# Optimization experiments

Hardware: AMD Instinct MI355X
Metric: run time of the kernel (lower is better)

## Reference

```python
import jax, jax.numpy as jnp
import numpy as np

H, W = 300, 400            # grid_size
RES = 0.1                  # resolution (m/pixel)
X0, X1 = -20.0, 20.0       # x_range
Y0, Y1 = -10.0, 30.0       # y_range
Z0, Z1 = -3.0, 4.0         # z_range
MAX_INT = 255.0            # max_intensity
N_MAX = 128.0              # density_normalize
K_SAMPLES = 512            # >= max Bresenham steps inside grid (diag <= 400)


def _rasterize_polyline(pts_xy):
    """DDA line rasterization of an ego-frame polyline -> [H, W] binary grid.
    Matches the Bresenham + 3x3 stamp (width 2 or 3 -> half_w=1) of the original."""
    px = jnp.trunc((pts_xy[:, 0] - X0) / RES)  # int() truncation as in original
    py = jnp.trunc((pts_xy[:, 1] - Y0) / RES)
    p = jnp.stack([px, py], axis=-1)           # [N, 2] pixel coords (float)
    a, b = p[:-1], p[1:]                        # segment endpoints [S, 2]

    def inb(q):
        return (q[:, 0] >= 0) & (q[:, 0] < W) & (q[:, 1] >= 0) & (q[:, 1] < H)

    valid = inb(a) | inb(b)                     # draw if either endpoint in bounds
    lo = jnp.array([0.0, 0.0], jnp.float32)
    hi = jnp.array([W - 1.0, H - 1.0], jnp.float32)
    a = jnp.clip(a, lo, hi)
    b = jnp.clip(b, lo, hi)

    dmax = jnp.max(jnp.abs(b - a), axis=-1)     # [S] major-axis length in pixels
    k = jnp.arange(K_SAMPLES, dtype=jnp.float32)
    t = jnp.minimum(k[None, :], dmax[:, None]) / jnp.maximum(dmax[:, None], 1.0)
    pts = a[:, None, :] + t[..., None] * (b - a)[:, None, :]   # [S, K, 2]
    pix = jnp.round(pts).astype(jnp.int32)

    offs = jnp.arange(-1, 2)                    # half_w = width//2 = 1 -> 3x3 stamp
    xs = pix[..., 0][..., None, None] + offs[:, None]          # [S, K, 3, 1]
    ys = pix[..., 1][..., None, None] + offs[None, :]          # [S, K, 1, 3]
    xs, ys = jnp.broadcast_arrays(xs, ys)
    val = jnp.broadcast_to(valid.astype(jnp.float32)[:, None, None, None], xs.shape)
    # out-of-bounds stamped pixels are dropped, as in the original bounds check
    return jnp.zeros((H, W), jnp.float32).at[ys, xs].max(val, mode="drop")


def _rasterize_lidar(points):
    """[N,4] (x,y,z,intensity) -> [3,H,W] (height, mean intensity, log density)."""
    x, y, z, inten = points[:, 0], points[:, 1], points[:, 2], points[:, 3]
    mask = (x >= X0) & (x < X1) & (y >= Y0) & (y < Y1)
    px = jnp.clip(((x - X0) / RES).astype(jnp.int32), 0, W - 1)
    py = jnp.clip(((y - Y0) / RES).astype(jnp.int32), 0, H - 1)
    w = mask.astype(jnp.float32)
    neg_inf = jnp.float32(-jnp.inf)

    hmax = jnp.full((H, W), neg_inf, jnp.float32).at[py, px].max(
        jnp.where(mask, z, neg_inf))
    hmax = jnp.where(jnp.isneginf(hmax), 0.0, hmax)  # empty cells -> 0 BEFORE norm

    isum = jnp.zeros((H, W), jnp.float32).at[py, px].add(inten * w)
    cnt = jnp.zeros((H, W), jnp.float32).at[py, px].add(w)
    imean = jnp.where(cnt > 0, isum / jnp.maximum(cnt, 1.0), 0.0)

    h = jnp.clip((hmax - Z0) / (Z1 - Z0), 0.0, 1.0)
    i = jnp.clip(imean / MAX_INT, 0.0, 1.0)
    d = jnp.clip(jnp.log1p(cnt) / jnp.log(1.0 + N_MAX), 0.0, 1.0)
    return jnp.stack([h, i, d])


def setup_inputs() -> dict:
    key = jax.random.key(0)
    k1, k2 = jax.random.split(key)
    # LiDAR: 4M points, slightly wider than the ROI so ~some get filtered
    u = jax.random.uniform(k1, (4_000_000, 4), dtype=jnp.float32)
    lo = jnp.array([-25.0, -15.0, -3.0, 0.0], jnp.float32)
    hi = jnp.array([25.0, 35.0, 4.0, 255.0], jnp.float32)
    lidar_points = lo + u * (hi - lo)
    # trajectory: smooth forward path in ego frame
    ty = jnp.linspace(0.0, 25.0, 50, dtype=jnp.float32)
    tx = 2.0 * jnp.sin(0.3 * ty)
    trajectory = jnp.stack([tx, ty], axis=-1)
    # OSM polyline: random walk in world frame (ego at origin)
    steps = 0.5 * jax.random.normal(k2, (2000, 2), dtype=jnp.float32)
    osm_coords = jnp.cumsum(steps, axis=0) + jnp.array([0.0, 10.0], jnp.float32)
    ego_pose = jnp.zeros((3,), jnp.float32)
    return {"lidar_points": lidar_points, "trajectory": trajectory,
            "osm_coords": osm_coords, "ego_pose": ego_pose}


def reference(lidar_points, trajectory, osm_coords, ego_pose):
    lidar_bev = _rasterize_lidar(lidar_points)                 # [3,H,W]
    traj_bev = _rasterize_polyline(trajectory)[None]           # [1,H,W]
    # world -> ego for OSM coords
    cy, sy = jnp.cos(-ego_pose[2]), jnp.sin(-ego_pose[2])
    d = osm_coords - ego_pose[:2]
    osm_ego = jnp.stack([d[:, 0] * cy - d[:, 1] * sy,
                         d[:, 0] * sy + d[:, 1] * cy], axis=-1)
    map_bev = _rasterize_polyline(osm_ego)[None]               # [1,H,W]
    return jnp.concatenate([lidar_bev, traj_bev, map_bev], axis=0)  # [5,H,W]
```

## Files before the change

### kernel.cpp

```cpp
#include <hip/hip_runtime.h>
#include <math.h>

#define GH 300
#define GW 400
#define GHW (GH * GW)

#define TCOLS 25
#define TROWS 19
#define T_TILES (TCOLS * TROWS)
#define B1 1024
#define Q 16
#define S2 4

__device__ __forceinline__ bool bin_point(float x, float y, int& px, int& py) {
    if (!(x >= -20.0f && x < 20.0f && y >= -10.0f && y < 30.0f)) return false;
    float qx = __fmul_rn(__fsub_rn(x, -20.0f), 10.0f);
    float qy = __fmul_rn(__fsub_rn(y, -10.0f), 10.0f);
    px = min(max((int)qx, 0), GW - 1);
    py = min(max((int)qy, 0), GH - 1);
    return true;
}

__device__ __forceinline__ void tile_prefix_wave0(const unsigned* src, unsigned* dst) {
    int lane = threadIdx.x;
    if (lane < 64) {
        unsigned run = 0;
        for (int c = 0; c < T_TILES; c += 64) {
            int idx = c + lane;
            unsigned v = (idx < T_TILES) ? src[idx] : 0u;
            unsigned orig = v;
#pragma unroll
            for (int d = 1; d < 64; d <<= 1) {
                unsigned u = __shfl_up(v, d, 64);
                if (lane >= d) v += u;
            }
            if (idx < T_TILES) dst[idx] = run + (v - orig);
            run += __shfl(v, 63, 64);
        }
        if (lane == 0) dst[T_TILES] = run;
    }
}

__device__ __forceinline__ bool make_record(float4 p, unsigned& rec, int& tile) {
    int px, py;
    if (!bin_point(p.x, p.y, px, py)) return false;
    tile = (py >> 4) * TCOLS + (px >> 4);
    int local = ((py & 15) << 4) | (px & 15);
    int z16 = min(max((int)rintf(__fmul_rn(__fadd_rn(p.z, 3.0f), 65535.0f / 7.0f)), 0), 65535);
    int i8 = min(max((int)rintf(p.w), 0), 255);
    rec = ((unsigned)z16 << 16) | ((unsigned)i8 << 8) | (unsigned)local;
    return true;
}

__global__ __launch_bounds__(256) void p1_kernel(const float4* __restrict__ pts, int n,
                                                 int per_block,
                                                 unsigned* __restrict__ staged,
                                                 unsigned* __restrict__ pref_t,
                                                 float* __restrict__ out) {
    __shared__ unsigned lbuf[256 * Q];
    __shared__ unsigned short ltile[256 * Q];
    __shared__ unsigned cnt[T_TILES];
    __shared__ unsigned pref[T_TILES + 1];
    __shared__ unsigned cur[T_TILES];
    for (int t = threadIdx.x; t < T_TILES; t += 256) cnt[t] = 0;
    float4* z4 = (float4*)(out + 3 * GHW);
    for (int j = blockIdx.x * 256 + (int)threadIdx.x; j < (2 * GHW) / 4; j += B1 * 256)
        z4[j] = make_float4(0.0f, 0.0f, 0.0f, 0.0f);
    __syncthreads();

    int start = blockIdx.x * per_block;
    int end = min(start + per_block, n);
    int nmine = 0;
    int i = start + (int)threadIdx.x;
    for (; i + 7 * 256 < end; i += 8 * 256) {
        float4 p[8];
#pragma unroll
        for (int j = 0; j < 8; ++j) p[j] = pts[i + j * 256];
#pragma unroll
        for (int j = 0; j < 8; ++j) {
            unsigned r;
            int tile;
            if (make_record(p[j], r, tile)) {
                lbuf[nmine * 256 + threadIdx.x] = r;
                ltile[nmine * 256 + threadIdx.x] = (unsigned short)tile;
                ++nmine;
                atomicAdd(&cnt[tile], 1u);
            }
        }
    }
    for (; i < end; i += 256) {
        unsigned r;
        int tile;
        if (make_record(pts[i], r, tile)) {
            lbuf[nmine * 256 + threadIdx.x] = r;
            ltile[nmine * 256 + threadIdx.x] = (unsigned short)tile;
            ++nmine;
            atomicAdd(&cnt[tile], 1u);
        }
    }
    __syncthreads();
    tile_prefix_wave0(cnt, pref);
    __syncthreads();
    for (int t = threadIdx.x; t < T_TILES; t += 256) cur[t] = pref[t];
    for (int t = threadIdx.x; t <= T_TILES; t += 256)
        pref_t[t * B1 + blockIdx.x] = pref[t];
    __syncthreads();
    size_t base = (size_t)blockIdx.x * (size_t)per_block;
    for (int j = 0; j < nmine; ++j) {
        unsigned r = lbuf[j * 256 + threadIdx.x];
        int tile = (int)ltile[j * 256 + threadIdx.x];
        unsigned pos = atomicAdd(&cur[tile], 1u);
        staged[base + pos] = r;
    }
}

__global__ __launch_bounds__(256) void p2a_kernel(const unsigned* __restrict__ staged,
                                                  const unsigned* __restrict__ pref_t,
                                                  int per_block,
                                                  unsigned* __restrict__ part_z,
                                                  unsigned long long* __restrict__ part_ic) {
    __shared__ unsigned zmax[256];
    __shared__ unsigned long long ic[256];
    int t = blockIdx.x / S2;
    int s = blockIdx.x % S2;
    zmax[threadIdx.x] = 0;
    ic[threadIdx.x] = 0;
    __syncthreads();
    int b = s * 256 + (int)threadIdx.x;
    unsigned ks = pref_t[t * B1 + b];
    unsigned ke = pref_t[(t + 1) * B1 + b];
    size_t base = (size_t)b * (size_t)per_block;
    for (unsigned k = ks; k < ke; ++k) {
        unsigned r = staged[base + k];
        int local = (int)(r & 255u);
        unsigned z16 = r >> 16;
        unsigned long long i8 = (r >> 8) & 255ull;
        atomicMax(&zmax[local], z16);
        atomicAdd(&ic[local], (1ull << 32) | i8);
    }
    __syncthreads();
    size_t pbase = (size_t)(t * S2 + s) * 256;
    part_z[pbase + threadIdx.x] = zmax[threadIdx.x];
    part_ic[pbase + threadIdx.x] = ic[threadIdx.x];
}

__device__ void do_poly_segment(int seg, const float2* __restrict__ traj, int ntraj,
                                const float2* __restrict__ osm, int nosm,
                                const float* __restrict__ ego, float* __restrict__ out) {
    int ntseg = ntraj - 1;
    int noseg = nosm - 1;
    if (seg >= ntseg + noseg) return;
    const float2* pts;
    float* out_ch;
    bool use_ego;
    if (seg < ntseg) {
        pts = traj + seg;
        out_ch = out + 3 * GHW;
        use_ego = false;
    } else {
        pts = osm + (seg - ntseg);
        out_ch = out + 4 * GHW;
        use_ego = true;
    }
    float2 P0 = pts[0];
    float2 P1 = pts[1];
    if (use_ego) {
        float yaw = ego[2];
        float cy = cosf(-yaw), sy = sinf(-yaw);
        float ex = ego[0], ey = ego[1];
        float d0x = __fsub_rn(P0.x, ex), d0y = __fsub_rn(P0.y, ey);
        float d1x = __fsub_rn(P1.x, ex), d1y = __fsub_rn(P1.y, ey);
        P0.x = __fsub_rn(__fmul_rn(d0x, cy), __fmul_rn(d0y, sy));
        P0.y = __fadd_rn(__fmul_rn(d0x, sy), __fmul_rn(d0y, cy));
        P1.x = __fsub_rn(__fmul_rn(d1x, cy), __fmul_rn(d1y, sy));
        P1.y = __fadd_rn(__fmul_rn(d1x, sy), __fmul_rn(d1y, cy));
    }
    double ax = trunc(__ddiv_rn(__dadd_rn((double)P0.x, 20.0), 0.1));
    double ay = trunc(__ddiv_rn(__dadd_rn((double)P0.y, 10.0), 0.1));
    double bx = trunc(__ddiv_rn(__dadd_rn((double)P1.x, 20.0), 0.1));
    double by = trunc(__ddiv_rn(__dadd_rn((double)P1.y, 10.0), 0.1));
    bool inA = (ax >= 0.0) && (ax < (double)GW) && (ay >= 0.0) && (ay < (double)GH);
    bool inB = (bx >= 0.0) && (bx < (double)GW) && (by >= 0.0) && (by < (double)GH);
    if (!(inA || inB)) return;
    ax = fmin(fmax(ax, 0.0), (double)(GW - 1));
    ay = fmin(fmax(ay, 0.0), (double)(GH - 1));
    bx = fmin(fmax(bx, 0.0), (double)(GW - 1));
    by = fmin(fmax(by, 0.0), (double)(GH - 1));
    double dx = __dsub_rn(bx, ax);
    double dy = __dsub_rn(by, ay);
    double dmax = fmax(fabs(dx), fabs(dy));
    double denom = fmax(dmax, 1.0);
    int kmax = (int)dmax;
    for (int k = 0; k <= kmax; ++k) {
        double t = __ddiv_rn(fmin((double)k, dmax), denom);
        double ptx = __dadd_rn(ax, __dmul_rn(t, dx));
        double pty = __dadd_rn(ay, __dmul_rn(t, dy));
        int cx = (int)rint(ptx);
        int cc = (int)rint(pty);
#pragma unroll
        for (int oy = -1; oy <= 1; ++oy) {
#pragma unroll
            for (int ox = -1; ox <= 1; ++ox) {
                int xx = cx + ox;
                int yy = cc + oy;
                if (xx < 0) xx += GW;
                if (yy < 0) yy += GH;
                if (xx >= 0 && xx < GW && yy >= 0 && yy < GH) {
                    out_ch[yy * GW + xx] = 1.0f;
                }
            }
        }
    }
}

__global__ __launch_bounds__(256) void p2b_kernel(const unsigned* __restrict__ part_z,
                                                  const unsigned long long* __restrict__ part_ic,
                                                  float* __restrict__ out,
                                                  const float2* __restrict__ traj, int ntraj,
                                                  const float2* __restrict__ osm, int nosm,
                                                  const float* __restrict__ ego) {
    if (blockIdx.x >= T_TILES) {
        int seg = (blockIdx.x - T_TILES) * 256 + (int)threadIdx.x;
        do_poly_segment(seg, traj, ntraj, osm, nosm, ego, out);
        return;
    }
    int t = blockIdx.x;
    int l = threadIdx.x;
    size_t pbase = (size_t)t * S2 * 256;
    unsigned zfin = 0;
    unsigned long long v = 0;
#pragma unroll
    for (int s = 0; s < S2; ++s) {
        zfin = max(zfin, part_z[pbase + s * 256 + l]);
        v += part_ic[pbase + s * 256 + l];
    }
    int trow = t / TCOLS, tcol = t % TCOLS;
    int gy = trow * 16 + (l >> 4);
    int gx = tcol * 16 + (l & 15);
    if (gy < GH) {
        const float inv7 = 1.0f / 7.0f;
        const float invlog129 = 1.0f / 4.8598124043616719e+00f;
        float h, ich, dd;
        if (v == 0) {
            h = fminf(fmaxf(__fmul_rn(3.0f, inv7), 0.0f), 1.0f);
            ich = 0.0f;
            dd = 0.0f;
        } else {
            unsigned cnt = (unsigned)(v >> 32);
            float sum8 = (float)(unsigned)(v & 0xFFFFFFFFull);
            h = fminf((float)zfin * (1.0f / 65535.0f), 1.0f);
            ich = fminf(__fdiv_rn(sum8, __fmul_rn((float)cnt, 255.0f)), 1.0f);
            dd = fminf(__fmul_rn(log1pf((float)cnt), invlog129), 1.0f);
        }
        int idx = gy * GW + gx;
        out[0 * GHW + idx] = h;
        out[1 * GHW + idx] = ich;
        out[2 * GHW + idx] = dd;
    }
}

__global__ __launch_bounds__(256) void polylines_kernel(const float2* __restrict__ traj,
                                                        int ntraj,
                                                        const float2* __restrict__ osm, int nosm,
                                                        const float* __restrict__ ego,
                                                        float* __restrict__ out) {
    int seg = blockIdx.x * 256 + (int)threadIdx.x;
    do_poly_segment(seg, traj, ntraj, osm, nosm, ego, out);
}

__global__ __launch_bounds__(256) void init_kernel(float* __restrict__ out) {
    int i = blockIdx.x * blockDim.x + threadIdx.x;
    if (i < GHW) {
        out[0 * GHW + i] = -INFINITY;
        out[1 * GHW + i] = 0.0f;
        out[2 * GHW + i] = 0.0f;
        out[3 * GHW + i] = 0.0f;
        out[4 * GHW + i] = 0.0f;
    }
}

__device__ __forceinline__ void atomicMaxFloat(float* addr, float val) {
    if (val >= 0.0f) {
        atomicMax((int*)addr, __float_as_int(val));
    } else {
        atomicMin((unsigned int*)addr, (unsigned int)__float_as_int(val));
    }
}

__global__ __launch_bounds__(256) void lidar_kernel(const float4* __restrict__ pts, int n,
                                                    float* __restrict__ out) {
    int i = blockIdx.x * blockDim.x + threadIdx.x;
    if (i >= n) return;
    float4 p = pts[i];
    int px, py;
    if (!bin_point(p.x, p.y, px, py)) return;
    int idx = py * GW + px;
    atomicMaxFloat(&out[0 * GHW + idx], p.z);
    atomicAdd(&out[1 * GHW + idx], p.w);
    atomicAdd(&out[2 * GHW + idx], 1.0f);
}

__global__ __launch_bounds__(256) void finalize_kernel(float* __restrict__ out) {
    int i = blockIdx.x * blockDim.x + threadIdx.x;
    if (i >= GHW) return;
    float hm = out[0 * GHW + i];
    float isum = out[1 * GHW + i];
    float c = out[2 * GHW + i];
    if (hm == -INFINITY) hm = 0.0f;
    const float inv7 = 1.0f / 7.0f;
    const float inv255 = 1.0f / 255.0f;
    const float invlog129 = 1.0f / 4.8598124043616719e+00f;
    float h = fminf(fmaxf(__fmul_rn(__fadd_rn(hm, 3.0f), inv7), 0.0f), 1.0f);
    float im = (c > 0.0f) ? __fdiv_rn(isum, fmaxf(c, 1.0f)) : 0.0f;
    float ich = fminf(fmaxf(__fmul_rn(im, inv255), 0.0f), 1.0f);
    float dd = fminf(fmaxf(__fmul_rn(log1pf(c), invlog129), 0.0f), 1.0f);
    out[0 * GHW + i] = h;
    out[1 * GHW + i] = ich;
    out[2 * GHW + i] = dd;
}

extern "C" void kernel_launch(void* const* d_in, const int* in_sizes, int n_in,
                              void* d_out, int out_size, void* d_ws, size_t ws_size,
                              hipStream_t stream) {
    const float* lidar = (const float*)d_in[0];
    const float* traj = (const float*)d_in[1];
    const float* osm = (const float*)d_in[2];
    const float* ego = (const float*)d_in[3];
    float* out = (float*)d_out;

    int n_lidar = in_sizes[0] / 4;
    int n_traj = in_sizes[1] / 2;
    int n_osm = in_sizes[2] / 2;
    int nseg = (n_traj - 1) + (n_osm - 1);
    int npb = (nseg + 255) / 256;

    int per_block = (n_lidar + B1 - 1) / B1;
    size_t staged_bytes = (size_t)B1 * (size_t)per_block * 4;
    size_t pic_bytes = (size_t)T_TILES * S2 * 256 * 8;
    size_t pz_bytes = (size_t)T_TILES * S2 * 256 * 4;
    size_t pref_bytes = (size_t)(T_TILES + 1) * B1 * 4;
    size_t need = staged_bytes + pic_bytes + pz_bytes + pref_bytes;

    if (ws_size >= need && per_block <= 256 * Q) {
        char* w = (char*)d_ws;
        unsigned* staged = (unsigned*)w;
        unsigned long long* part_ic = (unsigned long long*)(w + staged_bytes);
        unsigned* part_z = (unsigned*)(w + staged_bytes + pic_bytes);
        unsigned* pref_t = (unsigned*)(w + staged_bytes + pic_bytes + pz_bytes);

        p1_kernel<<<B1, 256, 0, stream>>>((const float4*)lidar, n_lidar, per_block, staged,
                                          pref_t, out);
        p2a_kernel<<<T_TILES * S2, 256, 0, stream>>>(staged, pref_t, per_block, part_z, part_ic);
        p2b_kernel<<<T_TILES + npb, 256, 0, stream>>>(part_z, part_ic, out,
                                                      (const float2*)traj, n_traj,
                                                      (const float2*)osm, n_osm, ego);
    } else {
        init_kernel<<<(GHW + 255) / 256, 256, 0, stream>>>(out);
        lidar_kernel<<<(n_lidar + 255) / 256, 256, 0, stream>>>((const float4*)lidar, n_lidar,
                                                                out);
        finalize_kernel<<<(GHW + 255) / 256, 256, 0, stream>>>(out);
        polylines_kernel<<<(nseg + 255) / 256, 256, 0, stream>>>((const float2*)traj, n_traj,
                                                                 (const float2*)osm, n_osm, ego,
                                                                 out);
    }
}
```

Measured before the change: 148.2 us.

## Fuse tile accumulation and finalize into one kernel, drop partial buffers

Merges the per-tile shared-memory accumulation kernel (p2a) into the finalize kernel (p2b). Each 256-thread block now walks all 1024 source block ranges for its tile, four per thread with interleaved loads, and finalizes directly from shared memory. This removes one kernel launch and the global round trip of the partial z/ic buffers. In exchange there are 4x fewer blocks doing the accumulation, so less parallelism and longer per-thread loops.

```diff
diff --git a/kernel.cpp b/kernel.cpp
--- a/kernel.cpp
+++ b/kernel.cpp
@@ -10,7 +10,6 @@
 #define T_TILES (TCOLS * TROWS)
 #define B1 1024
 #define Q 16
-#define S2 4
 
 __device__ __forceinline__ bool bin_point(float x, float y, int& px, int& py) {
     if (!(x >= -20.0f && x < 20.0f && y >= -10.0f && y < 30.0f)) return false;
@@ -112,36 +111,6 @@
         unsigned pos = atomicAdd(&cur[tile], 1u);
         staged[base + pos] = r;
     }
-}
-
-__global__ __launch_bounds__(256) void p2a_kernel(const unsigned* __restrict__ staged,
-                                                  const unsigned* __restrict__ pref_t,
-                                                  int per_block,
-                                                  unsigned* __restrict__ part_z,
-                                                  unsigned long long* __restrict__ part_ic) {
-    __shared__ unsigned zmax[256];
-    __shared__ unsigned long long ic[256];
-    int t = blockIdx.x / S2;
-    int s = blockIdx.x % S2;
-    zmax[threadIdx.x] = 0;
-    ic[threadIdx.x] = 0;
-    __syncthreads();
-    int b = s * 256 + (int)threadIdx.x;
-    unsigned ks = pref_t[t * B1 + b];
-    unsigned ke = pref_t[(t + 1) * B1 + b];
-    size_t base = (size_t)b * (size_t)per_block;
-    for (unsigned k = ks; k < ke; ++k) {
-        unsigned r = staged[base + k];
-        int local = (int)(r & 255u);
-        unsigned z16 = r >> 16;
-        unsigned long long i8 = (r >> 8) & 255ull;
-        atomicMax(&zmax[local], z16);
-        atomicAdd(&ic[local], (1ull << 32) | i8);
-    }
-    __syncthreads();
-    size_t pbase = (size_t)(t * S2 + s) * 256;
-    part_z[pbase + threadIdx.x] = zmax[threadIdx.x];
-    part_ic[pbase + threadIdx.x] = ic[threadIdx.x];
 }
 
 __device__ void do_poly_segment(int seg, const float2* __restrict__ traj, int ntraj,
@@ -213,27 +182,61 @@
     }
 }
 
-__global__ __launch_bounds__(256) void p2b_kernel(const unsigned* __restrict__ part_z,
-                                                  const unsigned long long* __restrict__ part_ic,
-                                                  float* __restrict__ out,
-                                                  const float2* __restrict__ traj, int ntraj,
-                                                  const float2* __restrict__ osm, int nosm,
-                                                  const float* __restrict__ ego) {
+__global__ __launch_bounds__(256) void p2_kernel(const unsigned* __restrict__ staged,
+                                                 const unsigned* __restrict__ pref_t,
+                                                 int per_block,
+                                                 float* __restrict__ out,
+                                                 const float2* __restrict__ traj, int ntraj,
+                                                 const float2* __restrict__ osm, int nosm,
+                                                 const float* __restrict__ ego) {
     if (blockIdx.x >= T_TILES) {
         int seg = (blockIdx.x - T_TILES) * 256 + (int)threadIdx.x;
         do_poly_segment(seg, traj, ntraj, osm, nosm, ego, out);
         return;
     }
+    __shared__ unsigned zmax[256];
+    __shared__ unsigned long long ic[256];
     int t = blockIdx.x;
     int l = threadIdx.x;
-    size_t pbase = (size_t)t * S2 * 256;
-    unsigned zfin = 0;
-    unsigned long long v = 0;
-#pragma unroll
-    for (int s = 0; s < S2; ++s) {
-        zfin = max(zfin, part_z[pbase + s * 256 + l]);
-        v += part_ic[pbase + s * 256 + l];
-    }
+    zmax[l] = 0;
+    ic[l] = 0;
+    __syncthreads();
+
+    unsigned ks[4], ke[4];
+    size_t base[4];
+#pragma unroll
+    for (int s = 0; s < 4; ++s) {
+        int b = s * 256 + l;
+        ks[s] = pref_t[t * B1 + b];
+        ke[s] = pref_t[(t + 1) * B1 + b];
+        base[s] = (size_t)b * (size_t)per_block;
+    }
+    for (;;) {
+        unsigned r[4];
+        bool any = false;
+#pragma unroll
+        for (int s = 0; s < 4; ++s) {
+            if (ks[s] < ke[s]) {
+                r[s] = staged[base[s] + ks[s]];
+                any = true;
+            }
+        }
+        if (!any) break;
+#pragma unroll
+        for (int s = 0; s < 4; ++s) {
+            if (ks[s] < ke[s]) {
+                unsigned rr = r[s];
+                int local = (int)(rr & 255u);
+                atomicMax(&zmax[local], rr >> 16);
+                atomicAdd(&ic[local], (1ull << 32) | ((rr >> 8) & 255ull));
+                ++ks[s];
+            }
+        }
+    }
+    __syncthreads();
+
+    unsigned zfin = zmax[l];
+    unsigned long long v = ic[l];
     int trow = t / TCOLS, tcol = t % TCOLS;
     int gy = trow * 16 + (l >> 4);
     int gx = tcol * 16 + (l & 15);
@@ -336,24 +339,19 @@
 
     int per_block = (n_lidar + B1 - 1) / B1;
     size_t staged_bytes = (size_t)B1 * (size_t)per_block * 4;
-    size_t pic_bytes = (size_t)T_TILES * S2 * 256 * 8;
-    size_t pz_bytes = (size_t)T_TILES * S2 * 256 * 4;
     size_t pref_bytes = (size_t)(T_TILES + 1) * B1 * 4;
-    size_t need = staged_bytes + pic_bytes + pz_bytes + pref_bytes;
+    size_t need = staged_bytes + pref_bytes;
 
     if (ws_size >= need && per_block <= 256 * Q) {
         char* w = (char*)d_ws;
         unsigned* staged = (unsigned*)w;
-        unsigned long long* part_ic = (unsigned long long*)(w + staged_bytes);
-        unsigned* part_z = (unsigned*)(w + staged_bytes + pic_bytes);
-        unsigned* pref_t = (unsigned*)(w + staged_bytes + pic_bytes + pz_bytes);
+        unsigned* pref_t = (unsigned*)(w + staged_bytes);
 
         p1_kernel<<<B1, 256, 0, stream>>>((const float4*)lidar, n_lidar, per_block, staged,
                                           pref_t, out);
-        p2a_kernel<<<T_TILES * S2, 256, 0, stream>>>(staged, pref_t, per_block, part_z, part_ic);
-        p2b_kernel<<<T_TILES + npb, 256, 0, stream>>>(part_z, part_ic, out,
-                                                      (const float2*)traj, n_traj,
-                                                      (const float2*)osm, n_osm, ego);
+        p2_kernel<<<T_TILES + npb, 256, 0, stream>>>(staged, pref_t, per_block, out,
+                                                     (const float2*)traj, n_traj,
+                                                     (const float2*)osm, n_osm, ego);
     } else {
         init_kernel<<<(GHW + 255) / 256, 256, 0, stream>>>(out);
         lidar_kernel<<<(n_lidar + 255) / 256, 256, 0, stream>>>((const float4*)lidar, n_lidar,
```

Result: slower. 171.9 us (+16.0%).
